# Performance work log

Hardware: AMD Instinct MI355X
Metric: run time of the kernel (lower is better)

Reference implementation:

```python
import jax, jax.numpy as jnp
import numpy as np

B, N, D = 2, 2048, 1024
H, WS = 16, 128  # num_heads, window_size
DH = D // H
HALF = WS // 2  # window is [i-HALF, i+HALF] inclusive -> 129 keys interior


def setup_inputs() -> dict:
    key = jax.random.key(0)
    ks = jax.random.split(key, 5)
    return {
        "x": jax.random.normal(ks[0], (B, N, D), dtype=jnp.float32),
        "Wqkv": jax.random.normal(ks[1], (D, 3 * D), dtype=jnp.float32) * 0.02,
        "bqkv": jax.random.normal(ks[2], (3 * D,), dtype=jnp.float32) * 0.02,
        "Wout": jax.random.normal(ks[3], (D, D), dtype=jnp.float32) * 0.02,
        "bout": jax.random.normal(ks[4], (D,), dtype=jnp.float32) * 0.02,
    }


def reference(x, Wqkv, bqkv, Wout, bout):
    b, n, d = x.shape
    scale = DH ** -0.5
    qkv = x @ Wqkv + bqkv  # [b, n, 3d]
    q, k, v = jnp.split(qkv, 3, axis=-1)
    # [b, n, d] -> [b, h, n, dh]
    def heads(t):
        return t.reshape(b, n, H, DH).transpose(0, 2, 1, 3)
    q, k, v = heads(q), heads(k), heads(v)
    scores = jnp.einsum("bhid,bhjd->bhij", q, k) * scale  # [b, h, n, n]
    # per-token window [max(0,i-HALF), min(n,i+HALF+1)) == |i-j| <= HALF
    idx = jnp.arange(n)
    band = jnp.abs(idx[:, None] - idx[None, :]) <= HALF  # [n, n]
    neg = jnp.asarray(jnp.finfo(scores.dtype).min, scores.dtype)
    scores = jnp.where(band[None, None], scores, neg)
    attn = jax.nn.softmax(scores, axis=-1)
    out = jnp.einsum("bhij,bhjd->bhid", attn, v)  # [b, h, n, dh]
    out = out.transpose(0, 2, 1, 3).reshape(b, n, d)
    return out @ Wout + bout
```

## Files before the change

kernel.cpp:

```cpp
#include <hip/hip_runtime.h>
#include <hip/hip_bf16.h>
#include <cstdint>
#include <cstddef>

#define BB 2
#define NN 2048
#define DD 1024
#define HH 16
#define DHH 64
#define SCALE 0.125f

typedef _Float16 f16x8 __attribute__((ext_vector_type(8)));
typedef _Float16 f16x4 __attribute__((ext_vector_type(4)));
typedef float f32x4 __attribute__((ext_vector_type(4)));

#define AS1(p) ((__attribute__((address_space(1))) void*)(p))
#define AS3(p) ((__attribute__((address_space(3))) void*)(p))

__global__ __launch_bounds__(256) void prep(const float* __restrict__ x, _Float16* __restrict__ x_h,
                                            const float* __restrict__ Wqkv, _Float16* __restrict__ Wqkv_t,
                                            const float* __restrict__ Wout, _Float16* __restrict__ Wout_t) {
    __shared__ float tile[32][33];
    int bx = blockIdx.x, tid = threadIdx.x;
    if (bx < 2048) {
        int i = bx * 2048 + tid * 8;
        f32x4 a = *(const f32x4*)(x + i);
        f32x4 b = *(const f32x4*)(x + i + 4);
        f16x8 o;
        o[0] = (_Float16)a[0]; o[1] = (_Float16)a[1]; o[2] = (_Float16)a[2]; o[3] = (_Float16)a[3];
        o[4] = (_Float16)b[0]; o[5] = (_Float16)b[1]; o[6] = (_Float16)b[2]; o[7] = (_Float16)b[3];
        *(f16x8*)(x_h + i) = o;
        return;
    }
    const float* in; _Float16* out; int C, tc, tr;
    if (bx < 5120) { int t = bx - 2048; C = 3 * DD; in = Wqkv; out = Wqkv_t; tc = t % 96; tr = t / 96; }
    else           { int t = bx - 5120; C = DD;     in = Wout; out = Wout_t; tc = t % 32; tr = t / 32; }
    int R = DD;
    int txx = tid & 31, ty = tid >> 5;
    int r0 = tr * 32, c0 = tc * 32;
#pragma unroll
    for (int i = 0; i < 32; i += 8)
        tile[ty + i][txx] = in[(size_t)(r0 + ty + i) * C + (c0 + txx)];
    __syncthreads();
#pragma unroll
    for (int i = 0; i < 32; i += 8)
        out[(size_t)(c0 + ty + i) * R + (r0 + txx)] = (_Float16)tile[txx][ty + i];
}

template <bool SWAP, int MT>
__device__ __forceinline__ void gemm_kloop(const _Float16* __restrict__ gA,
                                           const _Float16* __restrict__ gB,
                                           _Float16* lA, _Float16* lB,
                                           const _Float16* As, const _Float16* Bs,
                                           int wm, int wn, int llo, int lhi, int K,
                                           f32x4 acc[][MT > 4 ? MT : 4]) {
    for (int k0 = 0; k0 < K; k0 += 64) {
        __syncthreads();
#pragma unroll
        for (int p = 0; p < MT; ++p)
            __builtin_amdgcn_global_load_lds(AS1(gA + (size_t)p * 8 * K + k0), AS3(lA + p * 512), 16, 0, 0);
#pragma unroll
        for (int p = 0; p < 4; ++p)
            __builtin_amdgcn_global_load_lds(AS1(gB + (size_t)p * 8 * K + k0), AS3(lB + p * 512), 16, 0, 0);
        __syncthreads();

#pragma unroll
        for (int ks = 0; ks < 2; ++ks) {
            f16x8 af[MT], bf[4];
            int swz = (((ks * 4 + lhi) ^ (llo & 7)) * 8);
#pragma unroll
            for (int mt = 0; mt < MT; ++mt)
                af[mt] = *(const f16x8*)(As + (wm + mt * 16 + llo) * 64 + swz);
#pragma unroll
            for (int nt = 0; nt < 4; ++nt)
                bf[nt] = *(const f16x8*)(Bs + (wn + nt * 16 + llo) * 64 + swz);
            if (SWAP) {
#pragma unroll
                for (int nt = 0; nt < 4; ++nt)
#pragma unroll
                    for (int mt = 0; mt < MT; ++mt)
                        acc[nt][mt] = __builtin_amdgcn_mfma_f32_16x16x32_f16(bf[nt], af[mt], acc[nt][mt], 0, 0, 0);
            } else {
#pragma unroll
                for (int mt = 0; mt < MT; ++mt)
#pragma unroll
                    for (int nt = 0; nt < 4; ++nt)
                        acc[mt][nt] = __builtin_amdgcn_mfma_f32_16x16x32_f16(af[mt], bf[nt], acc[mt][nt], 0, 0, 0);
            }
        }
    }
}

__global__ __launch_bounds__(512, 2) void gemm_qkv(const _Float16* __restrict__ A,
                                                   const _Float16* __restrict__ Bt,
                                                   const float* __restrict__ bias,
                                                   _Float16* __restrict__ q_h,
                                                   _Float16* __restrict__ k_h,
                                                   _Float16* __restrict__ vt_h) {
    __shared__ __align__(16) _Float16 As[2 * 16384];
    __shared__ __align__(16) _Float16 Bs[2 * 12288];
    int id = blockIdx.x;
    int xcd = id & 7, jj = id >> 3;
    int mtile = (xcd >> 1) * 4 + (jj >> 3);
    int ntile = (xcd & 1) * 8 + (jj & 7);
    int bm = mtile * 256, bn = ntile * 192;

    int tid = threadIdx.x;
    int wave = tid >> 6, lane = tid & 63;
    int llo = lane & 15, lhi = lane >> 4;
    int wm = (wave >> 2) * 128, wn = (wave & 3) * 48;
    int l8 = lane >> 3;
    int gchunk = ((lane & 7) ^ l8) * 8;

    int rAu = wm + (wave & 3) * 16;
    const _Float16* gA = A + (size_t)(bm + rAu + l8) * DD + gchunk;
    _Float16* lA = As + rAu * 64 + lane * 8;
    const _Float16* gB = Bt + (size_t)(bn + wave * 8 + l8) * DD + gchunk;
    _Float16* lB = Bs + wave * 512 + lane * 8;

#define STA(H, C, T, U) __builtin_amdgcn_global_load_lds( \
        AS1(gA + (size_t)((H) * 64 + (C) * 8) * DD + (T) * 64), \
        AS3(lA + (U) * 16384 + ((H) * 64 + (C) * 8) * 64), 16, 0, 0)
#define STB(G, T, U) __builtin_amdgcn_global_load_lds( \
        AS1(gB + (size_t)((G) * 64) * DD + (T) * 64), \
        AS3(lB + (U) * 12288 + (G) * 4096), 16, 0, 0)
#define RDA(MT, KS, U) (*(const f16x8*)(As + (U) * 16384 + (wm + (MT) * 16 + llo) * 64 + ((((KS) * 4 + lhi) ^ (llo & 7)) * 8)))
#define RDB(NT, KS, U) (*(const f16x8*)(Bs + (U) * 12288 + (wn + (NT) * 16 + llo) * 64 + ((((KS) * 4 + lhi) ^ (llo & 7)) * 8)))
#define MM(MT, NT, KS) \
        acc[NT][MT] = __builtin_amdgcn_mfma_f32_16x16x32_f16(bf[NT][KS], af[(MT) & 3][KS], acc[NT][MT], 0, 0, 0)

    f32x4 acc[3][8] = {};
    f16x8 af[4][2], bf[3][2];

    STA(0, 0, 0, 0); STA(0, 1, 0, 0);
    STB(0, 0, 0); STB(1, 0, 0); STB(2, 0, 0);
    STA(1, 0, 0, 0); STA(1, 1, 0, 0);
    asm volatile("s_waitcnt vmcnt(2)" ::: "memory");
    __builtin_amdgcn_s_barrier();

#pragma unroll 1
    for (int t = 0; t < 15; ++t) {
        int u = t & 1, nu = u ^ 1;
#pragma unroll
        for (int mt = 0; mt < 4; ++mt) { af[mt][0] = RDA(mt, 0, u); af[mt][1] = RDA(mt, 1, u); }
#pragma unroll
        for (int nt = 0; nt < 3; ++nt) { bf[nt][0] = RDB(nt, 0, u); bf[nt][1] = RDB(nt, 1, u); }
        STA(0, 0, t + 1, nu); STA(0, 1, t + 1, nu);
        STB(0, t + 1, nu); STB(1, t + 1, nu); STB(2, t + 1, nu);
        __builtin_amdgcn_s_barrier();
        asm volatile("s_waitcnt lgkmcnt(0)" ::: "memory");
        __builtin_amdgcn_s_setprio(1);
#pragma unroll
        for (int ks = 0; ks < 2; ++ks)
#pragma unroll
            for (int mt = 0; mt < 4; ++mt) { MM(mt, 0, ks); MM(mt, 1, ks); MM(mt, 2, ks); }
        __builtin_amdgcn_s_setprio(0);
        asm volatile("s_waitcnt vmcnt(5)" ::: "memory");
        __builtin_amdgcn_s_barrier();
#pragma unroll
        for (int mt = 0; mt < 4; ++mt) { af[mt][0] = RDA(mt + 4, 0, u); af[mt][1] = RDA(mt + 4, 1, u); }
        STA(1, 0, t + 1, nu); STA(1, 1, t + 1, nu);
        __builtin_amdgcn_s_barrier();
        asm volatile("s_waitcnt lgkmcnt(0)" ::: "memory");
        __builtin_amdgcn_s_setprio(1);
#pragma unroll
        for (int ks = 0; ks < 2; ++ks)
#pragma unroll
            for (int mt = 4; mt < 8; ++mt) { MM(mt, 0, ks); MM(mt, 1, ks); MM(mt, 2, ks); }
        __builtin_amdgcn_s_setprio(0);
        asm volatile("s_waitcnt vmcnt(2)" ::: "memory");
        __builtin_amdgcn_s_barrier();
    }

    {
#pragma unroll
        for (int mt = 0; mt < 4; ++mt) { af[mt][0] = RDA(mt, 0, 1); af[mt][1] = RDA(mt, 1, 1); }
#pragma unroll
        for (int nt = 0; nt < 3; ++nt) { bf[nt][0] = RDB(nt, 0, 1); bf[nt][1] = RDB(nt, 1, 1); }
        asm volatile("s_waitcnt lgkmcnt(0)" ::: "memory");
        __builtin_amdgcn_s_setprio(1);
#pragma unroll
        for (int ks = 0; ks < 2; ++ks)
#pragma unroll
            for (int mt = 0; mt < 4; ++mt) { MM(mt, 0, ks); MM(mt, 1, ks); MM(mt, 2, ks); }
        __builtin_amdgcn_s_setprio(0);
        asm volatile("s_waitcnt vmcnt(0)" ::: "memory");
        __builtin_amdgcn_s_barrier();
#pragma unroll
        for (int mt = 0; mt < 4; ++mt) { af[mt][0] = RDA(mt + 4, 0, 1); af[mt][1] = RDA(mt + 4, 1, 1); }
        asm volatile("s_waitcnt lgkmcnt(0)" ::: "memory");
        __builtin_amdgcn_s_setprio(1);
#pragma unroll
        for (int ks = 0; ks < 2; ++ks)
#pragma unroll
            for (int mt = 4; mt < 8; ++mt) { MM(mt, 0, ks); MM(mt, 1, ks); MM(mt, 2, ks); }
        __builtin_amdgcn_s_setprio(0);
    }

    __builtin_amdgcn_s_barrier();
    _Float16* R = (wave < 4) ? (As + wave * 6144) : (Bs + (wave - 4) * 6144);
    int bq = bm >> 11;
    int nb = (bm & 2047) + wm;
    int cwb = bn + wn;

#pragma unroll
    for (int nt = 0; nt < 3; ++nt) {
        int fb = nt * 16 + lhi * 4;
        f32x4 b4 = *(const f32x4*)(bias + cwb + fb);
        int chunk = fb >> 3, off = fb & 7;
#pragma unroll
        for (int mt = 0; mt < 8; ++mt) {
            int t = mt * 16 + llo;
            f16x4 v4;
#pragma unroll
            for (int r = 0; r < 4; ++r) v4[r] = (_Float16)(acc[nt][mt][r] + b4[r]);
            *(f16x4*)(R + t * 48 + ((chunk + t) % 6) * 8 + off) = v4;
        }
    }
    asm volatile("s_waitcnt lgkmcnt(0)" ::: "memory");
#pragma unroll
    for (int it = 0; it < 16; ++it) {
        int t = it * 8 + l8;
        int c = lane & 7;
        if (c < 6) {
            int col = cwb + c * 8;
            int rg = col >> 10;
            if (rg < 2) {
                f16x8 v = *(const f16x8*)(R + t * 48 + ((c + t) % 6) * 8);
                _Float16* dst = rg ? k_h : q_h;
                *(f16x8*)(dst + (size_t)(bq * NN + nb + t) * DD + (col & 1023)) = v;
            }
        }
    }
#pragma unroll
    for (int nt = 0; nt < 3; ++nt) {
        int colbase = cwb + nt * 16;
        if ((colbase >> 10) == 2) {
            int fb = nt * 16 + lhi * 4;
            f32x4 b4 = *(const f32x4*)(bias + cwb + fb);
#pragma unroll
            for (int r = 0; r < 4; ++r) {
                int c1023 = (colbase + lhi * 4 + r) & 1023;
                int h = c1023 >> 6, dh = c1023 & 63;
                _Float16* vb = vt_h + ((size_t)((bq * HH + h) * DHH + dh)) * NN;
#pragma unroll
                for (int mt = 0; mt < 8; ++mt) {
                    int n = nb + mt * 16 + llo;
                    vb[n] = (_Float16)(acc[nt][mt][r] + b4[r]);
                }
            }
        }
    }
#undef STA
#undef STB
#undef RDA
#undef RDB
#undef MM
}

__global__ __launch_bounds__(256) void gemm_out(const _Float16* __restrict__ A,
                                                const _Float16* __restrict__ Bt,
                                                const float* __restrict__ bias,
                                                float* __restrict__ Cf) {
    const int K = DD, N = DD;
    __shared__ __align__(16) _Float16 As[128 * 64];
    __shared__ __align__(16) _Float16 Bs[128 * 64];
    int id = blockIdx.x;
    int xcd = id & 7, j = id >> 3;
    int bm = (xcd * 4 + (j >> 3)) * 128;
    int bn = (j & 7) * 128;
    int tid = threadIdx.x;
    int wave = tid >> 6, lane = tid & 63;
    int wm = (wave >> 1) * 64, wn = (wave & 1) * 64;
    int lhi = lane >> 4, llo = lane & 15;

    f32x4 acc[4][4] = {};

    int srow = wave * 32 + (lane >> 3);
    int scol = ((lane & 7) ^ (lane >> 3)) * 8;
    const _Float16* gA = A + (size_t)(bm + srow) * K + scol;
    const _Float16* gB = Bt + (size_t)(bn + srow) * K + scol;
    _Float16* lA = As + wave * 2048 + lane * 8;
    _Float16* lB = Bs + wave * 2048 + lane * 8;

    gemm_kloop<true, 4>(gA, gB, lA, lB, As, Bs, wm, wn, llo, lhi, K, acc);

#pragma unroll
    for (int nt = 0; nt < 4; ++nt) {
        int cbase = bn + wn + nt * 16 + lhi * 4;
        f32x4 b4 = *(const f32x4*)(bias + cbase);
#pragma unroll
        for (int mt = 0; mt < 4; ++mt) {
            int t = bm + wm + mt * 16 + llo;
            f32x4 v4;
#pragma unroll
            for (int r = 0; r < 4; ++r) v4[r] = acc[nt][mt][r] + b4[r];
            *(f32x4*)(Cf + (size_t)t * N + cbase) = v4;
        }
    }
}

#define KP 64
#define PP 200
#define VP 200
__global__ __launch_bounds__(256) void local_attn(const _Float16* __restrict__ q_h,
                                                  const _Float16* __restrict__ k_h,
                                                  const _Float16* __restrict__ vt_h,
                                                  _Float16* __restrict__ outh) {
    __shared__ __align__(16) _Float16 KsPs[64 * PP];
    __shared__ __align__(16) _Float16 Vt[64 * VP];
    _Float16* Ks = KsPs;
    _Float16* Ps = KsPs;
    int tid = threadIdx.x;
    int id = blockIdx.x;
    int xcd = id & 7, j = id >> 3;
    int i0 = (xcd * 4 + (j & 3)) * 64;
    int hb = j >> 2;
    int h = hb & 15, b = hb >> 4;

    int wave = tid >> 6, lane = tid & 63;
    int llo = lane & 15, lhi = lane >> 4;

    {
        int srow = lane >> 3;
        int chunk = ((lane & 7) ^ (lane >> 3)) * 8;
        const _Float16* kb = k_h + (size_t)(b * NN) * DD + h * DHH + chunk;
#pragma unroll
        for (int q = 0; q < 6; ++q) {
            int p = wave * 6 + q;
            int jj = i0 - 64 + p * 8 + srow;
            __builtin_amdgcn_global_load_lds(AS1(kb + (ptrdiff_t)jj * DD), AS3(Ks + p * 512 + lane * 8), 16, 0, 0);
        }
    }

    {
        const _Float16* vb = vt_h + (size_t)((b * HH + h) * DHH) * NN + (i0 - 64);
        for (int u = tid; u < 1536; u += 256) {
            int d = u / 24, c = u % 24;
            f16x8 vv = *(const f16x8*)(vb + (ptrdiff_t)d * NN + c * 8);
            *(f16x8*)(Vt + d * VP + c * 8) = vv;
        }
    }

    int qrow = wave * 16 + llo;
    int qi = i0 + qrow;
    const _Float16* qp = q_h + (size_t)(b * NN + qi) * DD + h * DHH;
    f16x8 qf0 = *(const f16x8*)(qp + lhi * 8);
    f16x8 qf1 = *(const f16x8*)(qp + 32 + lhi * 8);
    __syncthreads();

    float sc[12][4];
#pragma unroll
    for (int mt = 0; mt < 12; ++mt) {
        const _Float16* kr = Ks + (mt * 16 + llo) * 64;
        f16x8 kf0 = *(const f16x8*)(kr + ((lhi ^ (llo & 7)) * 8));
        f16x8 kf1 = *(const f16x8*)(kr + (((lhi + 4) ^ (llo & 7)) * 8));
        f32x4 a = {0.f, 0.f, 0.f, 0.f};
        a = __builtin_amdgcn_mfma_f32_16x16x32_f16(kf0, qf0, a, 0, 0, 0);
        a = __builtin_amdgcn_mfma_f32_16x16x32_f16(kf1, qf1, a, 0, 0, 0);
#pragma unroll
        for (int r = 0; r < 4; ++r) sc[mt][r] = a[r];
    }
    __syncthreads();

    float m = -1e30f;
#pragma unroll
    for (int mt = 0; mt < 12; ++mt)
#pragma unroll
        for (int r = 0; r < 4; ++r) {
            int sidx = mt * 16 + lhi * 4 + r;
            int jj = i0 - 64 + sidx;
            int dj = jj - qi;
            bool valid = (jj >= 0) && (jj < NN) && (dj <= 64) && (dj >= -64);
            float v = valid ? sc[mt][r] * SCALE : -1e30f;
            sc[mt][r] = v;
            m = fmaxf(m, v);
        }
    m = fmaxf(m, __shfl_xor(m, 16, 64));
    m = fmaxf(m, __shfl_xor(m, 32, 64));
    float l = 0.f;
#pragma unroll
    for (int mt = 0; mt < 12; ++mt)
#pragma unroll
        for (int r = 0; r < 4; ++r) {
            float e = __expf(sc[mt][r] - m);
            sc[mt][r] = e;
            l += e;
        }
    l += __shfl_xor(l, 16, 64);
    l += __shfl_xor(l, 32, 64);
    float invl = 1.f / l;

#pragma unroll
    for (int mt = 0; mt < 12; ++mt) {
        f16x4 pv;
#pragma unroll
        for (int r = 0; r < 4; ++r) pv[r] = (_Float16)(sc[mt][r] * invl);
        *(f16x4*)(Ps + qrow * PP + mt * 16 + lhi * 4) = pv;
    }
    __asm__ volatile("s_waitcnt lgkmcnt(0)" ::: "memory");

    f32x4 oacc[4] = {};
#pragma unroll
    for (int ks = 0; ks < 6; ++ks) {
        f16x8 pf = *(const f16x8*)(Ps + (wave * 16 + llo) * PP + ks * 32 + lhi * 8);
#pragma unroll
        for (int nt = 0; nt < 4; ++nt) {
            f16x8 vf = *(const f16x8*)(Vt + (nt * 16 + llo) * VP + ks * 32 + lhi * 8);
            oacc[nt] = __builtin_amdgcn_mfma_f32_16x16x32_f16(pf, vf, oacc[nt], 0, 0, 0);
        }
    }

    _Float16* orow = outh + (size_t)(b * NN) * DD + h * DHH;
#pragma unroll
    for (int nt = 0; nt < 4; ++nt)
#pragma unroll
        for (int r = 0; r < 4; ++r) {
            int q = wave * 16 + lhi * 4 + r;
            int d = nt * 16 + llo;
            orow[(size_t)(i0 + q) * DD + d] = (_Float16)oacc[nt][r];
        }
}

extern "C" void kernel_launch(void* const* d_in, const int* in_sizes, int n_in,
                              void* d_out, int out_size, void* d_ws, size_t ws_size,
                              hipStream_t stream) {
    const float* x    = (const float*)d_in[0];
    const float* Wqkv = (const float*)d_in[1];
    const float* bqkv = (const float*)d_in[2];
    const float* Wout = (const float*)d_in[3];
    const float* bout = (const float*)d_in[4];
    float* out = (float*)d_out;

    char* ws = (char*)d_ws;
    _Float16* x_h    = (_Float16*)(ws);
    _Float16* Wqkv_t = (_Float16*)(ws + (size_t)8  * 1024 * 1024);
    _Float16* Wout_t = (_Float16*)(ws + (size_t)14 * 1024 * 1024);
    _Float16* q_h    = (_Float16*)(ws + (size_t)16 * 1024 * 1024);
    _Float16* k_h    = (_Float16*)(ws + (size_t)24 * 1024 * 1024);
    _Float16* vt_h   = (_Float16*)(ws + (size_t)32 * 1024 * 1024);
    _Float16* attn_h = (_Float16*)(ws + (size_t)40 * 1024 * 1024);

    prep<<<6144, 256, 0, stream>>>(x, x_h, Wqkv, Wqkv_t, Wout, Wout_t);

    gemm_qkv<<<256, 512, 0, stream>>>(x_h, Wqkv_t, bqkv, q_h, k_h, vt_h);

    local_attn<<<1024, 256, 0, stream>>>(q_h, k_h, vt_h, attn_h);

    gemm_out<<<256, 256, 0, stream>>>(attn_h, Wout_t, bout, out);
}
```

Before: 150.9 us.

## Use 128-query attention tiles with per-wave diagonal key windows

The local attention kernel now handles 128 queries per block with 8 waves, so a 256-key window is shared across more queries. Each wave computes scores only for the 9 key tiles (144 keys) that overlap its 16 queries' band, rather than all 12 tiles. The PV product runs 5 k-steps over a wave-offset slice of V, with zero-padded P columns and V tail. The goal is less redundant MFMA and softmax work and less K/V reloading per query, at the cost of more shared memory per block and a different occupancy profile.

Result: faster. 145.1 us (median of 2 runs) (-3.8%).

```diff
diff --git a/kernel.cpp b/kernel.cpp
--- a/kernel.cpp
+++ b/kernel.cpp
@@ -300,22 +300,21 @@
     }
 }
 
-#define KP 64
-#define PP 200
-#define VP 200
-__global__ __launch_bounds__(256) void local_attn(const _Float16* __restrict__ q_h,
-                                                  const _Float16* __restrict__ k_h,
-                                                  const _Float16* __restrict__ vt_h,
-                                                  _Float16* __restrict__ outh) {
-    __shared__ __align__(16) _Float16 KsPs[64 * PP];
-    __shared__ __align__(16) _Float16 Vt[64 * VP];
+#define PP2 168
+#define VP2 280
+__global__ __launch_bounds__(512, 4) void local_attn(const _Float16* __restrict__ q_h,
+                                                     const _Float16* __restrict__ k_h,
+                                                     const _Float16* __restrict__ vt_h,
+                                                     _Float16* __restrict__ outh) {
+    __shared__ __align__(16) _Float16 KsPs[128 * PP2];
+    __shared__ __align__(16) _Float16 Vt[64 * VP2];
     _Float16* Ks = KsPs;
     _Float16* Ps = KsPs;
     int tid = threadIdx.x;
     int id = blockIdx.x;
     int xcd = id & 7, j = id >> 3;
-    int i0 = (xcd * 4 + (j & 3)) * 64;
-    int hb = j >> 2;
+    int i0 = (xcd * 2 + (j & 1)) * 128;
+    int hb = j >> 1;
     int h = hb & 15, b = hb >> 4;
 
     int wave = tid >> 6, lane = tid & 63;
@@ -326,8 +325,8 @@
         int chunk = ((lane & 7) ^ (lane >> 3)) * 8;
         const _Float16* kb = k_h + (size_t)(b * NN) * DD + h * DHH + chunk;
 #pragma unroll
-        for (int q = 0; q < 6; ++q) {
-            int p = wave * 6 + q;
+        for (int q = 0; q < 4; ++q) {
+            int p = wave * 4 + q;
             int jj = i0 - 64 + p * 8 + srow;
             __builtin_amdgcn_global_load_lds(AS1(kb + (ptrdiff_t)jj * DD), AS3(Ks + p * 512 + lane * 8), 16, 0, 0);
         }
@@ -335,10 +334,16 @@
 
     {
         const _Float16* vb = vt_h + (size_t)((b * HH + h) * DHH) * NN + (i0 - 64);
-        for (int u = tid; u < 1536; u += 256) {
-            int d = u / 24, c = u % 24;
+#pragma unroll
+        for (int u = tid; u < 2048; u += 512) {
+            int d = u >> 5, c = u & 31;
             f16x8 vv = *(const f16x8*)(vb + (ptrdiff_t)d * NN + c * 8);
-            *(f16x8*)(Vt + d * VP + c * 8) = vv;
+            *(f16x8*)(Vt + d * VP2 + c * 8) = vv;
+        }
+        if (tid < 192) {
+            int d = tid / 3, c = tid % 3;
+            f16x8 z = {};
+            *(f16x8*)(Vt + d * VP2 + 256 + c * 8) = z;
         }
     }
 
@@ -349,42 +354,42 @@
     f16x8 qf1 = *(const f16x8*)(qp + 32 + lhi * 8);
     __syncthreads();
 
-    float sc[12][4];
-#pragma unroll
-    for (int mt = 0; mt < 12; ++mt) {
-        const _Float16* kr = Ks + (mt * 16 + llo) * 64;
+    float sc[9][4];
+#pragma unroll
+    for (int mtl = 0; mtl < 9; ++mtl) {
+        const _Float16* kr = Ks + ((wave + mtl) * 16 + llo) * 64;
         f16x8 kf0 = *(const f16x8*)(kr + ((lhi ^ (llo & 7)) * 8));
         f16x8 kf1 = *(const f16x8*)(kr + (((lhi + 4) ^ (llo & 7)) * 8));
         f32x4 a = {0.f, 0.f, 0.f, 0.f};
         a = __builtin_amdgcn_mfma_f32_16x16x32_f16(kf0, qf0, a, 0, 0, 0);
         a = __builtin_amdgcn_mfma_f32_16x16x32_f16(kf1, qf1, a, 0, 0, 0);
 #pragma unroll
-        for (int r = 0; r < 4; ++r) sc[mt][r] = a[r];
+        for (int r = 0; r < 4; ++r) sc[mtl][r] = a[r];
     }
     __syncthreads();
 
     float m = -1e30f;
 #pragma unroll
-    for (int mt = 0; mt < 12; ++mt)
+    for (int mtl = 0; mtl < 9; ++mtl)
 #pragma unroll
         for (int r = 0; r < 4; ++r) {
-            int sidx = mt * 16 + lhi * 4 + r;
+            int sidx = (wave + mtl) * 16 + lhi * 4 + r;
             int jj = i0 - 64 + sidx;
             int dj = jj - qi;
             bool valid = (jj >= 0) && (jj < NN) && (dj <= 64) && (dj >= -64);
-            float v = valid ? sc[mt][r] * SCALE : -1e30f;
-            sc[mt][r] = v;
+            float v = valid ? sc[mtl][r] * SCALE : -1e30f;
+            sc[mtl][r] = v;
             m = fmaxf(m, v);
         }
     m = fmaxf(m, __shfl_xor(m, 16, 64));
     m = fmaxf(m, __shfl_xor(m, 32, 64));
     float l = 0.f;
 #pragma unroll
-    for (int mt = 0; mt < 12; ++mt)
+    for (int mtl = 0; mtl < 9; ++mtl)
 #pragma unroll
         for (int r = 0; r < 4; ++r) {
-            float e = __expf(sc[mt][r] - m);
-            sc[mt][r] = e;
+            float e = __expf(sc[mtl][r] - m);
+            sc[mtl][r] = e;
             l += e;
         }
     l += __shfl_xor(l, 16, 64);
@@ -392,21 +397,25 @@
     float invl = 1.f / l;
 
 #pragma unroll
-    for (int mt = 0; mt < 12; ++mt) {
+    for (int mtl = 0; mtl < 9; ++mtl) {
         f16x4 pv;
 #pragma unroll
-        for (int r = 0; r < 4; ++r) pv[r] = (_Float16)(sc[mt][r] * invl);
-        *(f16x4*)(Ps + qrow * PP + mt * 16 + lhi * 4) = pv;
+        for (int r = 0; r < 4; ++r) pv[r] = (_Float16)(sc[mtl][r] * invl);
+        *(f16x4*)(Ps + qrow * PP2 + mtl * 16 + lhi * 4) = pv;
+    }
+    {
+        f16x4 z4 = {};
+        *(f16x4*)(Ps + qrow * PP2 + 144 + lhi * 4) = z4;
     }
     __asm__ volatile("s_waitcnt lgkmcnt(0)" ::: "memory");
 
     f32x4 oacc[4] = {};
 #pragma unroll
-    for (int ks = 0; ks < 6; ++ks) {
-        f16x8 pf = *(const f16x8*)(Ps + (wave * 16 + llo) * PP + ks * 32 + lhi * 8);
+    for (int ks = 0; ks < 5; ++ks) {
+        f16x8 pf = *(const f16x8*)(Ps + qrow * PP2 + ks * 32 + lhi * 8);
 #pragma unroll
         for (int nt = 0; nt < 4; ++nt) {
-            f16x8 vf = *(const f16x8*)(Vt + (nt * 16 + llo) * VP + ks * 32 + lhi * 8);
+            f16x8 vf = *(const f16x8*)(Vt + (nt * 16 + llo) * VP2 + wave * 16 + ks * 32 + lhi * 8);
             oacc[nt] = __builtin_amdgcn_mfma_f32_16x16x32_f16(pf, vf, oacc[nt], 0, 0, 0);
         }
     }
@@ -445,7 +454,7 @@
 
     gemm_qkv<<<256, 512, 0, stream>>>(x_h, Wqkv_t, bqkv, q_h, k_h, vt_h);
 
-    local_attn<<<1024, 256, 0, stream>>>(q_h, k_h, vt_h, attn_h);
+    local_attn<<<512, 512, 0, stream>>>(q_h, k_h, vt_h, attn_h);
 
     gemm_out<<<256, 256, 0, stream>>>(attn_h, Wout_t, bout, out);
 }
```
